# Performance work log

Hardware: AMD Instinct MI355X
Metric: run time of the kernel (lower is better)

The kernel has to match this reference:

```python
import jax, jax.numpy as jnp
import numpy as np

NA = 3        # num anchors
NM = 32       # num prototype masks
NC = 80       # num classes
STRIDE = 8    # network stride
THRESH = 0.05 # conf threshold


def setup_inputs() -> dict:
    key = jax.random.key(0)
    nB, nH, nW = 16, 80, 80
    channels = NA * (5 + NC) + NA * NM  # 351
    output = jax.random.normal(key, (nB, channels, nH, nW), dtype=jnp.float32)
    # anchors already in output-grid units (pixel anchors / stride), shape [NA, 2] = (w, h)
    anchors = jnp.array([[1.25, 1.625], [2.0, 3.75], [4.125, 2.875]], dtype=jnp.float32)
    return {"output": output, "anchors": anchors}


def reference(output, anchors):
    nB, channels, nH, nW = output.shape
    nHW = nH * nW
    # split box head and mask-coefficient head
    box = output[:, :NA * (5 + NC)].reshape(nB, NA, 5 + NC, nHW)
    mask_out = output[:, NA * (5 + NC):].reshape(nB, NA, NM, nHW).transpose(0, 1, 3, 2)  # [nB,NA,nHW,NM]

    lin_y, lin_x = jnp.meshgrid(jnp.arange(nH, dtype=output.dtype),
                                jnp.arange(nW, dtype=output.dtype), indexing='ij')
    lin_x = lin_x.reshape(-1)
    lin_y = lin_y.reshape(-1)

    anchor_wh = anchors.reshape(1, NA, 2, 1)  # broadcast over [nB,NA,2,nHW]
    max_value = jnp.floor(jnp.log(jnp.asarray(1e35, output.dtype) / anchors.max() / STRIDE))

    xs = jax.nn.sigmoid(box[:, :, 0]) + lin_x                                   # [nB,NA,nHW]
    ys = jax.nn.sigmoid(box[:, :, 1]) + lin_y                                   # [nB,NA,nHW]
    wh = jnp.exp(jnp.minimum(box[:, :, 2:4], max_value)) * anchor_wh            # [nB,NA,2,nHW]
    obj = jax.nn.sigmoid(box[:, :, 4])                                          # [nB,NA,nHW]

    cls = jax.nn.softmax(box[:, :, 5:], axis=2)                                 # [nB,NA,NC,nHW]
    cls_max = cls.max(axis=2)
    cls_idx = cls.argmax(axis=2).astype(output.dtype)
    score = cls_max * obj                                                        # [nB,NA,nHW]

    keep = score > THRESH
    b, a, p = jnp.nonzero(keep)  # eager: data-dependent detection count N

    coords = jnp.stack([xs[b, a, p], ys[b, a, p], wh[b, a, 0, p], wh[b, a, 1, p]], axis=1) * STRIDE  # [N,4]
    mc = mask_out[b, a, p]                                                        # [N,NM]
    return jnp.concatenate([
        b[:, None].astype(output.dtype),
        coords,
        mc,
        score[b, a, p][:, None],
        cls_idx[b, a, p][:, None],
    ], axis=1)  # [N, 7+NM]
```

## Files before the change

### kernel.cpp

```cpp
#include <hip/hip_runtime.h>
#include <math.h>

#define NA 3
#define NM 32
#define NC 80
#define STRIDE_PX 8.0f
#define THRESH 0.05f
#define NB 16
#define NH 80
#define NW 80
#define NHW (NH * NW)
#define CH (NA * (5 + NC) + NA * NM)
#define BOXCH (NA * (5 + NC))
#define TOTAL (NB * NA * NHW)
#define BLK 256
#define NBLK (TOTAL / BLK)
#define ROWSZ (7 + NM)

__global__ __launch_bounds__(BLK) void pass1_kernel(
    const float* __restrict__ in, const float* __restrict__ anchors,
    float* __restrict__ vals, int* __restrict__ counts) {
  int g = blockIdx.x * BLK + threadIdx.x;
  int p = g % NHW;
  int a = (g / NHW) % NA;
  int b = g / (NA * NHW);

  const float* base = in + ((size_t)b * CH + (size_t)a * (5 + NC)) * NHW + p;

  float tx = base[0];
  float ty = base[(size_t)1 * NHW];
  float tw = base[(size_t)2 * NHW];
  float th = base[(size_t)3 * NHW];
  float tobj = base[(size_t)4 * NHW];

  float cl[NC];
  float m = -INFINITY;
  int idx = 0;
#pragma unroll
  for (int j = 0; j < NC; ++j) {
    cl[j] = base[(size_t)(5 + j) * NHW];
    if (cl[j] > m) { m = cl[j]; idx = j; }
  }
  float s = 0.f;
#pragma unroll
  for (int j = 0; j < NC; ++j) s += expf(cl[j] - m);

  float cls_max = 1.0f / s;
  float obj = 1.0f / (1.0f + expf(-tobj));
  float score = cls_max * obj;

  float amax = anchors[0];
#pragma unroll
  for (int j = 1; j < NA * 2; ++j) amax = fmaxf(amax, anchors[j]);
  float max_value = floorf(logf(1e35f / amax / STRIDE_PX));

  float aw = anchors[a * 2 + 0];
  float ah = anchors[a * 2 + 1];

  float xs = 1.0f / (1.0f + expf(-tx)) + (float)(p % NW);
  float ys = 1.0f / (1.0f + expf(-ty)) + (float)(p / NW);
  float w = expf(fminf(tw, max_value)) * aw;
  float h = expf(fminf(th, max_value)) * ah;

  float4 v0 = make_float4(xs, ys, w, h);
  float4 v1 = make_float4(score, (float)idx, 0.f, 0.f);
  float4* vp = (float4*)vals;
  vp[(size_t)g * 2 + 0] = v0;
  vp[(size_t)g * 2 + 1] = v1;

  bool keep = score > THRESH;
  unsigned long long ball = __ballot(keep);
  __shared__ int wc[BLK / 64];
  int lane = threadIdx.x & 63;
  int wv = threadIdx.x >> 6;
  if (lane == 0) wc[wv] = __popcll(ball);
  __syncthreads();
  if (threadIdx.x == 0) {
    int t = 0;
#pragma unroll
    for (int w2 = 0; w2 < BLK / 64; ++w2) t += wc[w2];
    counts[blockIdx.x] = t;
  }
}

__global__ __launch_bounds__(256) void scan_kernel(const int* __restrict__ counts,
                                                   int* __restrict__ offsets) {
  __shared__ int sh[2048];
  int t = threadIdx.x;
  for (int i = t; i < 2048; i += 256) sh[i] = (i < NBLK) ? counts[i] : 0;
  __syncthreads();
  for (int d = 1; d < 2048; d <<= 1) {
    int v[8];
#pragma unroll
    for (int k = 0; k < 8; ++k) {
      int i = t + k * 256;
      v[k] = (i >= d) ? sh[i - d] : 0;
    }
    __syncthreads();
#pragma unroll
    for (int k = 0; k < 8; ++k) sh[t + k * 256] += v[k];
    __syncthreads();
  }
  for (int i = t; i < NBLK; i += 256) offsets[i] = (i == 0) ? 0 : sh[i - 1];
}

__global__ __launch_bounds__(BLK) void pass3_kernel(
    const float* __restrict__ in, const float* __restrict__ vals,
    const int* __restrict__ offsets, float* __restrict__ out, int out_size) {
  int g = blockIdx.x * BLK + threadIdx.x;
  int p = g % NHW;
  int a = (g / NHW) % NA;
  int b = g / (NA * NHW);

  const float4* vp = (const float4*)vals;
  float4 v0 = vp[(size_t)g * 2 + 0];
  float4 v1 = vp[(size_t)g * 2 + 1];
  float score = v1.x;
  bool keep = score > THRESH;

  unsigned long long ball = __ballot(keep);
  int lane = threadIdx.x & 63;
  int wv = threadIdx.x >> 6;
  int lower = __popcll(ball & ((1ull << lane) - 1ull));
  __shared__ int wc[BLK / 64];
  if (lane == 0) wc[wv] = __popcll(ball);
  __syncthreads();
  int pre = 0;
  for (int w2 = 0; w2 < wv; ++w2) pre += wc[w2];

  if (keep) {
    int row = offsets[blockIdx.x] + pre + lower;
    if ((size_t)(row + 1) * ROWSZ <= (size_t)out_size) {
      float* o = out + (size_t)row * ROWSZ;
      o[0] = (float)b;
      o[1] = v0.x * STRIDE_PX;
      o[2] = v0.y * STRIDE_PX;
      o[3] = v0.z * STRIDE_PX;
      o[4] = v0.w * STRIDE_PX;
      const float* mbase = in + ((size_t)b * CH + BOXCH + (size_t)a * NM) * NHW + p;
#pragma unroll
      for (int mm = 0; mm < NM; ++mm) o[5 + mm] = mbase[(size_t)mm * NHW];
      o[5 + NM] = score;
      o[6 + NM] = v1.y;
    }
  }
}

extern "C" void kernel_launch(void* const* d_in, const int* in_sizes, int n_in,
                              void* d_out, int out_size, void* d_ws, size_t ws_size,
                              hipStream_t stream) {
  const float* in = (const float*)d_in[0];
  const float* anchors = (const float*)d_in[1];

  float* vals = (float*)d_ws;
  int* counts = (int*)((char*)d_ws + (size_t)TOTAL * 8 * 4);
  int* offsets = counts + NBLK;

  pass1_kernel<<<NBLK, BLK, 0, stream>>>(in, anchors, vals, counts);
  scan_kernel<<<1, 256, 0, stream>>>(counts, offsets);
  pass3_kernel<<<NBLK, BLK, 0, stream>>>(in, vals, offsets, (float*)d_out, out_size);
}
```

Measured before the change: 226.2 us.

## Fuse three-pass compaction into single kernel with decoupled look-back scan

Replaces the pass1/scan/pass3 pipeline with one kernel that computes detections and derives each block's output offset through a decoupled look-back prefix scan over global flags. This drops the intermediate vals buffer write and read and two kernel launches, adding a memset of the flag array in their place. The look-back spins on earlier blocks' flags, so it relies on blocks being scheduled in order and may serialize somewhat across blocks.

```diff
diff --git a/kernel.cpp b/kernel.cpp
--- a/kernel.cpp
+++ b/kernel.cpp
@@ -17,9 +17,13 @@
 #define NBLK (TOTAL / BLK)
 #define ROWSZ (7 + NM)
 
-__global__ __launch_bounds__(BLK) void pass1_kernel(
+#define FLAG_AGG  (1u << 30)
+#define FLAG_PREF (2u << 30)
+#define VAL_MASK  ((1u << 30) - 1u)
+
+__global__ __launch_bounds__(BLK) void fused_kernel(
     const float* __restrict__ in, const float* __restrict__ anchors,
-    float* __restrict__ vals, int* __restrict__ counts) {
+    float* __restrict__ out, int out_size, unsigned int* __restrict__ flags) {
   int g = blockIdx.x * BLK + threadIdx.x;
   int p = g % NHW;
   int a = (g / NHW) % NA;
@@ -49,11 +53,9 @@
   float obj = 1.0f / (1.0f + expf(-tobj));
   float score = cls_max * obj;
 
-  float amax = anchors[0];
-#pragma unroll
-  for (int j = 1; j < NA * 2; ++j) amax = fmaxf(amax, anchors[j]);
+  float amax = fmaxf(fmaxf(fmaxf(anchors[0], anchors[1]), fmaxf(anchors[2], anchors[3])),
+                     fmaxf(anchors[4], anchors[5]));
   float max_value = floorf(logf(1e35f / amax / STRIDE_PX));
-
   float aw = anchors[a * 2 + 0];
   float ah = anchors[a * 2 + 1];
 
@@ -62,86 +64,60 @@
   float w = expf(fminf(tw, max_value)) * aw;
   float h = expf(fminf(th, max_value)) * ah;
 
-  float4 v0 = make_float4(xs, ys, w, h);
-  float4 v1 = make_float4(score, (float)idx, 0.f, 0.f);
-  float4* vp = (float4*)vals;
-  vp[(size_t)g * 2 + 0] = v0;
-  vp[(size_t)g * 2 + 1] = v1;
-
   bool keep = score > THRESH;
-  unsigned long long ball = __ballot(keep);
-  __shared__ int wc[BLK / 64];
-  int lane = threadIdx.x & 63;
-  int wv = threadIdx.x >> 6;
-  if (lane == 0) wc[wv] = __popcll(ball);
-  __syncthreads();
-  if (threadIdx.x == 0) {
-    int t = 0;
-#pragma unroll
-    for (int w2 = 0; w2 < BLK / 64; ++w2) t += wc[w2];
-    counts[blockIdx.x] = t;
-  }
-}
-
-__global__ __launch_bounds__(256) void scan_kernel(const int* __restrict__ counts,
-                                                   int* __restrict__ offsets) {
-  __shared__ int sh[2048];
-  int t = threadIdx.x;
-  for (int i = t; i < 2048; i += 256) sh[i] = (i < NBLK) ? counts[i] : 0;
-  __syncthreads();
-  for (int d = 1; d < 2048; d <<= 1) {
-    int v[8];
-#pragma unroll
-    for (int k = 0; k < 8; ++k) {
-      int i = t + k * 256;
-      v[k] = (i >= d) ? sh[i - d] : 0;
-    }
-    __syncthreads();
-#pragma unroll
-    for (int k = 0; k < 8; ++k) sh[t + k * 256] += v[k];
-    __syncthreads();
-  }
-  for (int i = t; i < NBLK; i += 256) offsets[i] = (i == 0) ? 0 : sh[i - 1];
-}
-
-__global__ __launch_bounds__(BLK) void pass3_kernel(
-    const float* __restrict__ in, const float* __restrict__ vals,
-    const int* __restrict__ offsets, float* __restrict__ out, int out_size) {
-  int g = blockIdx.x * BLK + threadIdx.x;
-  int p = g % NHW;
-  int a = (g / NHW) % NA;
-  int b = g / (NA * NHW);
-
-  const float4* vp = (const float4*)vals;
-  float4 v0 = vp[(size_t)g * 2 + 0];
-  float4 v1 = vp[(size_t)g * 2 + 1];
-  float score = v1.x;
-  bool keep = score > THRESH;
-
   unsigned long long ball = __ballot(keep);
   int lane = threadIdx.x & 63;
   int wv = threadIdx.x >> 6;
   int lower = __popcll(ball & ((1ull << lane) - 1ull));
   __shared__ int wc[BLK / 64];
+  __shared__ int s_off;
   if (lane == 0) wc[wv] = __popcll(ball);
   __syncthreads();
   int pre = 0;
-  for (int w2 = 0; w2 < wv; ++w2) pre += wc[w2];
+#pragma unroll
+  for (int i = 0; i < BLK / 64; ++i)
+    if (i < wv) pre += wc[i];
+
+  if (threadIdx.x == 0) {
+    unsigned agg = (unsigned)(wc[0] + wc[1] + wc[2] + wc[3]);
+    unsigned bid = blockIdx.x;
+    if (bid == 0) {
+      __hip_atomic_store(&flags[0], FLAG_PREF | agg, __ATOMIC_RELEASE,
+                         __HIP_MEMORY_SCOPE_AGENT);
+      s_off = 0;
+    } else {
+      __hip_atomic_store(&flags[bid], FLAG_AGG | agg, __ATOMIC_RELEASE,
+                         __HIP_MEMORY_SCOPE_AGENT);
+      unsigned run = 0;
+      int j = (int)bid - 1;
+      while (true) {
+        unsigned f = __hip_atomic_load(&flags[j], __ATOMIC_ACQUIRE,
+                                       __HIP_MEMORY_SCOPE_AGENT);
+        if (f & FLAG_PREF) { run += f & VAL_MASK; break; }
+        if (f & FLAG_AGG)  { run += f & VAL_MASK; --j; }
+      }
+      __hip_atomic_store(&flags[bid], FLAG_PREF | (run + agg), __ATOMIC_RELEASE,
+                         __HIP_MEMORY_SCOPE_AGENT);
+      s_off = (int)run;
+    }
+  }
+  __syncthreads();
+  int row0 = s_off;
 
   if (keep) {
-    int row = offsets[blockIdx.x] + pre + lower;
+    int row = row0 + pre + lower;
     if ((size_t)(row + 1) * ROWSZ <= (size_t)out_size) {
       float* o = out + (size_t)row * ROWSZ;
       o[0] = (float)b;
-      o[1] = v0.x * STRIDE_PX;
-      o[2] = v0.y * STRIDE_PX;
-      o[3] = v0.z * STRIDE_PX;
-      o[4] = v0.w * STRIDE_PX;
+      o[1] = xs * STRIDE_PX;
+      o[2] = ys * STRIDE_PX;
+      o[3] = w * STRIDE_PX;
+      o[4] = h * STRIDE_PX;
       const float* mbase = in + ((size_t)b * CH + BOXCH + (size_t)a * NM) * NHW + p;
 #pragma unroll
       for (int mm = 0; mm < NM; ++mm) o[5 + mm] = mbase[(size_t)mm * NHW];
       o[5 + NM] = score;
-      o[6 + NM] = v1.y;
+      o[6 + NM] = (float)idx;
     }
   }
 }
@@ -152,11 +128,8 @@
   const float* in = (const float*)d_in[0];
   const float* anchors = (const float*)d_in[1];
 
-  float* vals = (float*)d_ws;
-  int* counts = (int*)((char*)d_ws + (size_t)TOTAL * 8 * 4);
-  int* offsets = counts + NBLK;
+  unsigned int* flags = (unsigned int*)d_ws;
 
-  pass1_kernel<<<NBLK, BLK, 0, stream>>>(in, anchors, vals, counts);
-  scan_kernel<<<1, 256, 0, stream>>>(counts, offsets);
-  pass3_kernel<<<NBLK, BLK, 0, stream>>>(in, vals, offsets, (float*)d_out, out_size);
+  hipMemsetAsync(flags, 0, NBLK * sizeof(unsigned int), stream);
+  fused_kernel<<<NBLK, BLK, 0, stream>>>(in, anchors, (float*)d_out, out_size, flags);
 }
```

After: 626.5 us. 2.77x slower.
